# Performance work log

Measured on AMD Instinct MI355X. Metric: run time of the kernel, lower is better.

Reference implementation:

```python
import jax, jax.numpy as jnp
import numpy as np

K = 3          # opt.k: number of nearest SOM nodes each point is assigned to
SOM_M = 256    # opt.node_num (16x16 SOM grid)


def _point_resnet(x, ws, bs):
    # SO-Net PointResNet: stack of 1x1 conv (relu) layers; the LAST layer takes
    # concat(prev_out, input) as a residual skip connection.
    out = x
    n = len(ws)
    for i in range(n):
        inp = jnp.concatenate([out, x], axis=1) if i == n - 1 else out
        out = jax.nn.relu(jnp.einsum('oc,bcn->bon', ws[i], inp) + bs[i][None, :, None])
    return out


def _encoder(x, sn, node, fp_ws, fp_bs, fn_ws, fn_bs):
    B, _, N = x.shape
    M = node.shape[2]
    xd = jax.lax.stop_gradient(x)      # torch used x.data throughout SOM logic
    nd = jax.lax.stop_gradient(node)
    # squared distances point->node: B,N,M
    x2 = jnp.sum(xd * xd, axis=1)
    n2 = jnp.sum(nd * nd, axis=1)
    cross = jnp.einsum('bcn,bcm->bnm', xd, nd)
    d2 = x2[:, :, None] + n2[:, None, :] - 2.0 * cross
    _, knn_idx = jax.lax.top_k(-d2, K)                 # B,N,K nearest SOM nodes
    min_idx = jnp.transpose(knn_idx, (0, 2, 1)).reshape(B, K * N)  # B,kN (k-major, matches x_stack)
    x_stack = jnp.tile(x, (1, 1, K))                   # B,3,kN
    xs_d = jax.lax.stop_gradient(x_stack)
    # mask_row_sum (counts per node) and masked sum == one-hot mask multiply in the original
    counts = jax.vmap(lambda s: jax.ops.segment_sum(jnp.ones(s.shape, jnp.float32), s, num_segments=SOM_M))(min_idx)  # B,M
    sums = jax.vmap(lambda d, s: jax.ops.segment_sum(d, s, num_segments=SOM_M))(jnp.transpose(xs_d, (0, 2, 1)), min_idx)  # B,M,3
    cluster_mean = jnp.transpose(sums, (0, 2, 1)) / (counts[:, None, :] + 1e-5)  # B,3,M (new som_node)
    # centers: per-point gather of its assigned node (sum(mask*node) over M)
    centers = jnp.take_along_axis(cluster_mean, min_idx[:, None, :], axis=2)     # B,3,kN
    x_dec = jax.lax.stop_gradient(x_stack - centers)   # .detach() in original
    first = _point_resnet(x_dec, fp_ws, fp_bs)         # B,384,kN
    # index_max + gather: per (b,c,node) max over assigned points; empty nodes -> point index 0
    node_max = jax.vmap(lambda d, s: jax.ops.segment_max(d, s, num_segments=SOM_M))(jnp.transpose(first, (0, 2, 1)), min_idx)  # B,M,C
    node_max = jnp.transpose(node_max, (0, 2, 1))      # B,C,M
    has_pts = counts > 0                               # mask_row_max
    fallback = first[:, :, 0:1]                        # gather index 0 for empty nodes
    masked_max = jnp.where(has_pts[:, None, :], node_max, fallback)  # B,384,M
    final_in = jnp.concatenate([cluster_mean, masked_max], axis=1)   # B,387,M
    final = _point_resnet(final_in, fn_ws, fn_bs)      # B,1024,M
    return jnp.max(final, axis=2)                      # B,1024 global feature


def setup_inputs() -> dict:
    key = jax.random.key(0)
    ks = jax.random.split(key, 24)
    B, N, M = 8, 4096, SOM_M
    inp = {
        'x': jax.random.normal(ks[0], (B, 3, N), jnp.float32),
        'sn': jax.random.normal(ks[1], (B, 3, N), jnp.float32),
        'node': jax.random.normal(ks[2], (B, 3, M), jnp.float32),
        'node_knn_I': jax.random.randint(ks[3], (B, M, 1), 0, M),
    }
    fp_dims = [(3, 64), (64, 128), (128, 256), (256 + 3, 384)]
    fn_dims = [(387, 512), (512, 512), (512, 768), (768 + 387, 1024)]
    i = 4
    for j, (cin, cout) in enumerate(fp_dims):
        inp[f'fp_w{j}'] = jax.random.normal(ks[i], (cout, cin), jnp.float32) * np.float32(np.sqrt(2.0 / cin)); i += 1
        inp[f'fp_b{j}'] = jnp.zeros((cout,), jnp.float32)
    for j, (cin, cout) in enumerate(fn_dims):
        inp[f'fn_w{j}'] = jax.random.normal(ks[i], (cout, cin), jnp.float32) * np.float32(np.sqrt(2.0 / cin)); i += 1
        inp[f'fn_b{j}'] = jnp.zeros((cout,), jnp.float32)
    return inp


def reference(x, sn, node, node_knn_I,
              fp_w0, fp_b0, fp_w1, fp_b1, fp_w2, fp_b2, fp_w3, fp_b3,
              fn_w0, fn_b0, fn_w1, fn_b1, fn_w2, fn_b2, fn_w3, fn_b3):
    fp_ws = [fp_w0, fp_w1, fp_w2, fp_w3]
    fp_bs = [fp_b0, fp_b1, fp_b2, fp_b3]
    fn_ws = [fn_w0, fn_w1, fn_w2, fn_w3]
    fn_bs = [fn_b0, fn_b1, fn_b2, fn_b3]
    # node_knn_I only used when som_k >= 2 (KNNModule); som_k=1 here.
    return _encoder(x, sn, node, fp_ws, fp_bs, fn_ws, fn_bs)
```

## Files before the change

### kernel.cpp

```cpp
#include <hip/hip_runtime.h>
#include <math.h>

#define B_   8
#define N_   4096
#define M_   256
#define KNN_ 3

#define OFF_COUNTS   0
#define OFF_SUMS     2048
#define OFF_CM       8192
#define OFF_NODEMAX  14336
#define OFF_H0       14336
#define OFF_FIRST0   800768
#define OFF_CURSOR   803840
#define ZERO_COUNT   805888
#define OFF_OFFS     805888
#define OFF_KNN      807944
#define OFF_CAT      807944
#define OFF_SORTED   906248
#define OFF_MSORT    1004552
#define OFF_FIN2     2020360
#define OFF_H1       2020360
#define OFF_WBF      2544648
#define OFF_W3X      3661832
#define O_W0 0
#define O_W1 2048
#define O_W2 10240
#define O_W3 43008
#define O_V0 153600
#define O_V1 366592
#define O_V2 628736
#define O_V3 1021952
#define W_TOTAL 2234368

typedef short  bf16x8 __attribute__((ext_vector_type(8)));
typedef float  f32x4  __attribute__((ext_vector_type(4)));
typedef float  f32x16 __attribute__((ext_vector_type(16)));

__device__ __forceinline__ unsigned short f2b(float f) {
    unsigned u = __float_as_uint(f);
    return (unsigned short)((u + 0x7FFFu + ((u >> 16) & 1u)) >> 16);
}
__device__ __forceinline__ unsigned cvt2(float lo, float hi) {
    unsigned r;
    asm("v_cvt_pk_bf16_f32 %0, %1, %2" : "=v"(r) : "v"(lo), "v"(hi));
    return r;
}
__device__ __forceinline__ f32x16 zero16() {
    f32x16 z;
    #pragma unroll
    for (int i = 0; i < 16; i++) z[i] = 0.f;
    return z;
}

__global__ __launch_bounds__(256) void knn_setup(
        const float* __restrict__ x, const float* __restrict__ node,
        int* __restrict__ knn, float* __restrict__ counts, float* __restrict__ sums,
        const float* s0, const float* s1, const float* s2, const float* s3,
        const float* s4, const float* s5, const float* s6, const float* s7,
        unsigned short* __restrict__ dst, float* __restrict__ w3x) {
    __shared__ float nd0[M_], nd1[M_], nd2[M_], nn2[M_];
    int t = threadIdx.x;
    if (blockIdx.x < 128) {
        int b = blockIdx.x >> 4, xblk = blockIdx.x & 15;
        {
            float c0 = node[(b * 3 + 0) * M_ + t];
            float c1 = node[(b * 3 + 1) * M_ + t];
            float c2 = node[(b * 3 + 2) * M_ + t];
            nd0[t] = c0; nd1[t] = c1; nd2[t] = c2;
            nn2[t] = c0 * c0 + c1 * c1 + c2 * c2;
        }
        __syncthreads();
        int n = xblk * 256 + t;
        float x0 = x[(b * 3 + 0) * N_ + n];
        float x1 = x[(b * 3 + 1) * N_ + n];
        float x2 = x[(b * 3 + 2) * N_ + n];
        float xx = x0 * x0 + x1 * x1 + x2 * x2;
        float d0 = 1e30f, d1 = 1e30f, d2b = 1e30f;
        int i0 = 0, i1 = 0, i2 = 0;
        for (int m = 0; m < M_; m++) {
            float cross = x0 * nd0[m] + x1 * nd1[m] + x2 * nd2[m];
            float d = xx + nn2[m] - 2.f * cross;
            bool c0 = d < d0, c1 = d < d1, c2 = d < d2b;
            d2b = c1 ? d1 : (c2 ? d : d2b);
            i2  = c1 ? i1 : (c2 ? m : i2);
            d1  = c0 ? d0 : (c1 ? d : d1);
            i1  = c0 ? i0 : (c1 ? m : i1);
            d0  = c0 ? d  : d0;
            i0  = c0 ? m  : i0;
        }
        int base = (b * N_ + n) * 3;
        knn[base + 0] = i0; knn[base + 1] = i1; knn[base + 2] = i2;
        int mm[3] = {i0, i1, i2};
        #pragma unroll
        for (int k = 0; k < 3; k++) {
            int m = mm[k];
            atomicAdd(&counts[b * M_ + m], 1.f);
            atomicAdd(&sums[(b * M_ + m) * 3 + 0], x0);
            atomicAdd(&sums[(b * M_ + m) * 3 + 1], x1);
            atomicAdd(&sums[(b * M_ + m) * 3 + 2], x2);
        }
    } else {
        int i = (blockIdx.x - 128) * 256 + t;
        int st = (gridDim.x - 128) * 256;
        for (int j = i; j < 1536; j += st) {
            int ch = j >> 2, c = j & 3;
            w3x[j] = (c < 3) ? s3[ch * 259 + 256 + c] : 0.f;
        }
        for (; i < W_TOTAL; i += st) {
            const float* src; int base, cin, cinp;
            if      (i < O_W1) { src = s0; base = O_W0; cin = 3;    cinp = 32; }
            else if (i < O_W2) { src = s1; base = O_W1; cin = 64;   cinp = 64; }
            else if (i < O_W3) { src = s2; base = O_W2; cin = 128;  cinp = 128; }
            else if (i < O_V0) { src = s3; base = O_W3; cin = 259;  cinp = 288; }
            else if (i < O_V1) { src = s4; base = O_V0; cin = 387;  cinp = 416; }
            else if (i < O_V2) { src = s5; base = O_V1; cin = 512;  cinp = 512; }
            else if (i < O_V3) { src = s6; base = O_V2; cin = 512;  cinp = 512; }
            else               { src = s7; base = O_V3; cin = 1155; cinp = 1184; }
            int loc = i - base;
            int co = loc / cinp, k = loc - co * cinp;
            dst[i] = (k < cin) ? f2b(src[co * cin + k]) : (unsigned short)0;
        }
    }
}

__global__ __launch_bounds__(256) void cmean_scan(const float* __restrict__ counts,
        const float* __restrict__ sums, float* __restrict__ cm, int* __restrict__ offs) {
    __shared__ int tmp[256];
    int t = threadIdx.x, b = blockIdx.x;
    float cnt = counts[b * M_ + t];
    float inv = 1.f / (cnt + 1e-5f);
    #pragma unroll
    for (int c = 0; c < 3; c++)
        cm[(b * 3 + c) * M_ + t] = sums[(b * M_ + t) * 3 + c] * inv;
    int v = (int)cnt;
    tmp[t] = v;
    __syncthreads();
    for (int off = 1; off < 256; off <<= 1) {
        int u = (t >= off) ? tmp[t - off] : 0;
        __syncthreads();
        tmp[t] += u;
        __syncthreads();
    }
    offs[b * 257 + t] = tmp[t] - v;
    if (t == 255) offs[b * 257 + 256] = tmp[255];
}

__global__ __launch_bounds__(256) void scatter(const int* __restrict__ knn,
        const int* __restrict__ offs, int* __restrict__ cursor,
        int* __restrict__ sorted, int* __restrict__ msort) {
    int g = blockIdx.x * 256 + threadIdx.x;
    int b = g / (KNN_ * N_), j = g % (KNN_ * N_);
    int n = j & (N_ - 1), k = j >> 12;
    int m = knn[(b * N_ + n) * 3 + k];
    int pos = atomicAdd(&cursor[b * M_ + m], 1);
    int dst = offs[b * 257 + m] + pos;
    sorted[b * (KNN_ * N_) + dst] = j;
    msort[b * (KNN_ * N_) + dst] = m;
}

template<int KS, int INS, int OUTS, int CTW>
__device__ __forceinline__ void layerB(const unsigned short* __restrict__ Wg,
        const float* __restrict__ bias, const unsigned short* actin,
        unsigned short* actout, int wave, int lane) {
    int r = lane & 15, g = lane >> 4;
    bf16x8 bfr[4][KS];
    #pragma unroll
    for (int pt = 0; pt < 4; pt++) {
        const unsigned short* arow = actin + (pt * 16 + r) * INS + g * 8;
        #pragma unroll
        for (int ks = 0; ks < KS; ks++)
            bfr[pt][ks] = *(const bf16x8*)(arow + ks * 32);
    }
    #pragma unroll
    for (int c = 0; c < CTW; c++) {
        int ct = wave * CTW + c;
        const unsigned short* wrow = Wg + (ct * 16 + r) * (KS * 32) + g * 8;
        f32x4 acc[4];
        #pragma unroll
        for (int pt = 0; pt < 4; pt++) acc[pt] = (f32x4){0.f, 0.f, 0.f, 0.f};
        #pragma unroll
        for (int ks = 0; ks < KS; ks++) {
            bf16x8 wv = *(const bf16x8*)(wrow + ks * 32);
            #pragma unroll
            for (int pt = 0; pt < 4; pt++)
                acc[pt] = __builtin_amdgcn_mfma_f32_16x16x32_bf16(wv, bfr[pt][ks], acc[pt], 0, 0, 0);
        }
        f32x4 b4 = *(const f32x4*)(bias + ct * 16 + g * 4);
        #pragma unroll
        for (int pt = 0; pt < 4; pt++) {
            uint2 s;
            s.x = cvt2(fmaxf(acc[pt][0] + b4[0], 0.f), fmaxf(acc[pt][1] + b4[1], 0.f));
            s.y = cvt2(fmaxf(acc[pt][2] + b4[2], 0.f), fmaxf(acc[pt][3] + b4[3], 0.f));
            *(uint2*)(actout + (pt * 16 + r) * OUTS + ct * 16 + g * 4) = s;
        }
    }
}

__global__ __launch_bounds__(256, 3) void mlp1m(
        const float* __restrict__ x, const float* __restrict__ cm,
        const int* __restrict__ sorted, const int* __restrict__ msort,
        const unsigned short* __restrict__ wb, const float4* __restrict__ w3x,
        const float* __restrict__ bb0, const float* __restrict__ bb1,
        const float* __restrict__ bb2, const float* __restrict__ bb3,
        float* __restrict__ node_max, float* __restrict__ first0) {
    __shared__ __align__(16) char smem[50688];
    unsigned short* inb = (unsigned short*)smem;
    unsigned short* a1  = (unsigned short*)smem;
    unsigned short* a0  = (unsigned short*)(smem + 16896);
    unsigned short* cat = (unsigned short*)(smem + 16896);
    __shared__ float4 xdf[64];
    __shared__ int segm[65], segstart[66];
    __shared__ int nseg, p0loc;
    int t = threadIdx.x, b = blockIdx.y, lane = t & 63, wave = t >> 6;
    int e0 = blockIdx.x * 64;
    for (int e = t; e < 1280; e += 256) ((unsigned*)inb)[e] = 0u;
    __syncthreads();
    if (t < 64) {
        int p = t;
        if (p == 0) p0loc = -1;
        int j = sorted[b * 12288 + e0 + p];
        int m = msort[b * 12288 + e0 + p];
        int n = j & (N_ - 1);
        float xd0 = x[(b * 3 + 0) * N_ + n] - cm[(b * 3 + 0) * M_ + m];
        float xd1 = x[(b * 3 + 1) * N_ + n] - cm[(b * 3 + 1) * M_ + m];
        float xd2 = x[(b * 3 + 2) * N_ + n] - cm[(b * 3 + 2) * M_ + m];
        xdf[p] = make_float4(xd0, xd1, xd2, 0.f);
        inb[p * 40 + 0] = f2b(xd0);
        inb[p * 40 + 1] = f2b(xd1);
        inb[p * 40 + 2] = f2b(xd2);
        int prev = __shfl_up(m, 1);
        bool flag = (p == 0) || (m != prev);
        unsigned long long mk = __ballot(flag);
        int sid = __popcll(mk & ((1ull << p) - 1ull));
        if (flag) { segstart[sid] = p; segm[sid] = m; }
        if (p == 63) { int ns2 = __popcll(mk); nseg = ns2; segstart[ns2] = 64; }
        if (j == 0) p0loc = p;
    }
    __syncthreads();
    layerB<1, 40, 72, 1>(wb + O_W0, bb0, inb, a0, wave, lane);
    __syncthreads();
    layerB<2, 72, 132, 2>(wb + O_W1, bb1, a0, a1, wave, lane);
    __syncthreads();
    layerB<4, 132, 264, 4>(wb + O_W2, bb2, a1, cat, wave, lane);
    __syncthreads();
    int l31 = lane & 31, half = lane >> 5;
    f32x16 acc[6];
    #pragma unroll
    for (int q = 0; q < 6; q++) acc[q] = zero16();
    {
        const unsigned short* arow0 = cat + l31 * 264 + half * 8;
        const unsigned short* arow1 = cat + (32 + l31) * 264 + half * 8;
        const unsigned short* wrowb = wb + O_W3 + (wave * 96 + l31) * 288 + half * 8;
        #pragma unroll
        for (int ks = 0; ks < 16; ks++) {
            bf16x8 aA = *(const bf16x8*)(arow0 + ks * 16);
            bf16x8 aB = *(const bf16x8*)(arow1 + ks * 16);
            #pragma unroll
            for (int c3 = 0; c3 < 3; c3++) {
                bf16x8 wv = *(const bf16x8*)(wrowb + c3 * 32 * 288 + ks * 16);
                acc[c3 * 2 + 0] = __builtin_amdgcn_mfma_f32_32x32x16_bf16(aA, wv, acc[c3 * 2 + 0], 0, 0, 0);
                acc[c3 * 2 + 1] = __builtin_amdgcn_mfma_f32_32x32x16_bf16(aB, wv, acc[c3 * 2 + 1], 0, 0, 0);
            }
        }
    }
    int ns = nseg, p0l = p0loc;
    float bias3[3]; float4 wx3[3];
    #pragma unroll
    for (int c3 = 0; c3 < 3; c3++) {
        bias3[c3] = bb3[(wave * 3 + c3) * 32 + l31];
        wx3[c3]   = w3x[(wave * 3 + c3) * 32 + l31];
    }
    #pragma unroll
    for (int ph = 0; ph < 2; ph++) {
        #pragma unroll
        for (int rg = 0; rg < 16; rg++) {
            int row = ph * 32 + (rg & 3) + 8 * (rg >> 2) + 4 * half;
            float4 xv = xdf[row];
            #pragma unroll
            for (int c3 = 0; c3 < 3; c3++) {
                float s = acc[c3 * 2 + ph][rg] + bias3[c3]
                        + wx3[c3].x * xv.x + wx3[c3].y * xv.y + wx3[c3].z * xv.z;
                acc[c3 * 2 + ph][rg] = fmaxf(s, 0.f);
            }
        }
    }
    if (p0l >= 0) {
        #pragma unroll
        for (int ph = 0; ph < 2; ph++)
            #pragma unroll
            for (int rg = 0; rg < 16; rg++) {
                int row = ph * 32 + (rg & 3) + 8 * (rg >> 2) + 4 * half;
                if (row == p0l) {
                    #pragma unroll
                    for (int c3 = 0; c3 < 3; c3++)
                        first0[b * 384 + (wave * 3 + c3) * 32 + l31] = acc[c3 * 2 + ph][rg];
                }
            }
    }
    for (int s = 0; s < ns; s++) {
        int s0 = segstart[s], s1 = segstart[s + 1];
        float m0 = 0.f, m1 = 0.f, m2 = 0.f;
        if (s0 < 32) {
            #pragma unroll
            for (int rg = 0; rg < 16; rg++) {
                int row = (rg & 3) + 8 * (rg >> 2) + 4 * half;
                bool in = (row >= s0) && (row < s1);
                m0 = fmaxf(m0, in ? acc[0][rg] : 0.f);
                m1 = fmaxf(m1, in ? acc[2][rg] : 0.f);
                m2 = fmaxf(m2, in ? acc[4][rg] : 0.f);
            }
        }
        if (s1 > 32) {
            #pragma unroll
            for (int rg = 0; rg < 16; rg++) {
                int row = 32 + (rg & 3) + 8 * (rg >> 2) + 4 * half;
                bool in = (row >= s0) && (row < s1);
                m0 = fmaxf(m0, in ? acc[1][rg] : 0.f);
                m1 = fmaxf(m1, in ? acc[3][rg] : 0.f);
                m2 = fmaxf(m2, in ? acc[5][rg] : 0.f);
            }
        }
        m0 = fmaxf(m0, __shfl_xor(m0, 32));
        m1 = fmaxf(m1, __shfl_xor(m1, 32));
        m2 = fmaxf(m2, __shfl_xor(m2, 32));
        if (lane < 32) {
            float* dstp = &node_max[(size_t)(b * M_ + segm[s]) * 384 + wave * 96];
            atomicMax((int*)(dstp + l31),      __float_as_int(m0));
            atomicMax((int*)(dstp + 32 + l31), __float_as_int(m1));
            atomicMax((int*)(dstp + 64 + l31), __float_as_int(m2));
        }
    }
}

__global__ void build_fin2(const float* __restrict__ cm, const float* __restrict__ counts,
                           const float* __restrict__ nmax, const float* __restrict__ first0,
                           unsigned short* __restrict__ fin2, unsigned short* __restrict__ cat) {
    int tot = 2048 * 416;
    int i = blockIdx.x * blockDim.x + threadIdx.x;
    int st = gridDim.x * blockDim.x;
    for (; i < tot; i += st) {
        int n = i / 416, ch = i - n * 416;
        int b = n >> 8, m = n & 255;
        float v = 0.f;
        if (ch < 3) v = cm[(b * 3 + ch) * M_ + m];
        else if (ch < 387)
            v = (counts[n] > 0.f) ? nmax[(size_t)n * 384 + (ch - 3)]
                                  : first0[b * 384 + (ch - 3)];
        unsigned short u = f2b(v);
        fin2[n * 416 + ch] = u;
        cat[(size_t)n * 1184 + 768 + ch] = u;
    }
}

template<int KS, int CTQ>
__global__ __launch_bounds__(256, 2) void nlayer4(const unsigned short* __restrict__ W,
        const float* __restrict__ bias, const unsigned short* __restrict__ actin,
        unsigned short* __restrict__ actout, int outs) {
    int wave = threadIdx.x >> 6, lane = threadIdx.x & 63;
    int id = blockIdx.x * 4 + wave;
    int nt = id / CTQ, cq = id - nt * CTQ;
    int r = lane & 15, g = lane >> 4;
    const unsigned short* arow = actin + (size_t)(nt * 16 + r) * (KS * 32) + g * 8;
    bf16x8 afr[KS];
    #pragma unroll
    for (int ks = 0; ks < KS; ks++) afr[ks] = *(const bf16x8*)(arow + ks * 32);
    const unsigned short* w0 = W + (cq * 64 + r) * (KS * 32) + g * 8;
    f32x4 acc[4];
    #pragma unroll
    for (int c = 0; c < 4; c++) acc[c] = (f32x4){0.f, 0.f, 0.f, 0.f};
    #pragma unroll
    for (int ks = 0; ks < KS; ks++) {
        #pragma unroll
        for (int c = 0; c < 4; c++) {
            bf16x8 wv = *(const bf16x8*)(w0 + c * 16 * KS * 32 + ks * 32);
            acc[c] = __builtin_amdgcn_mfma_f32_16x16x32_bf16(wv, afr[ks], acc[c], 0, 0, 0);
        }
    }
    #pragma unroll
    for (int c = 0; c < 4; c++) {
        f32x4 b4 = *(const f32x4*)(bias + cq * 64 + c * 16 + g * 4);
        uint2 s;
        s.x = cvt2(fmaxf(acc[c][0] + b4[0], 0.f), fmaxf(acc[c][1] + b4[1], 0.f));
        s.y = cvt2(fmaxf(acc[c][2] + b4[2], 0.f), fmaxf(acc[c][3] + b4[3], 0.f));
        *(uint2*)(actout + (size_t)(nt * 16 + r) * outs + cq * 64 + c * 16 + g * 4) = s;
    }
}

__global__ __launch_bounds__(256) void nlayer_max_s(const unsigned short* __restrict__ W,
        const float* __restrict__ bias, const unsigned short* __restrict__ actin,
        float* __restrict__ out) {
    int wave = threadIdx.x >> 6, lane = threadIdx.x & 63;
    int id = blockIdx.x * 4 + wave;
    int nt = id >> 5, cp = id & 31;
    int r = lane & 15, g = lane >> 4;
    const unsigned short* arow = actin + (size_t)(nt * 16 + r) * 1184 + g * 8;
    const unsigned short* w0 = W + (size_t)(cp * 32 + r) * 1184 + g * 8;
    const unsigned short* w1 = w0 + 16 * 1184;
    f32x4 a0 = {0.f, 0.f, 0.f, 0.f}, a1 = {0.f, 0.f, 0.f, 0.f};
    #pragma unroll 4
    for (int ks = 0; ks < 37; ks++) {
        bf16x8 av = *(const bf16x8*)(arow + ks * 32);
        a0 = __builtin_amdgcn_mfma_f32_16x16x32_bf16(*(const bf16x8*)(w0 + ks * 32), av, a0, 0, 0, 0);
        a1 = __builtin_amdgcn_mfma_f32_16x16x32_bf16(*(const bf16x8*)(w1 + ks * 32), av, a1, 0, 0, 0);
    }
    int b = nt >> 4;
    #pragma unroll
    for (int c = 0; c < 2; c++) {
        f32x4 acc = c ? a1 : a0;
        f32x4 b4 = *(const f32x4*)(bias + cp * 32 + c * 16 + g * 4);
        #pragma unroll
        for (int i = 0; i < 4; i++) {
            float v = fmaxf(acc[i] + b4[i], 0.f);
            v = fmaxf(v, __shfl_xor(v, 1));
            v = fmaxf(v, __shfl_xor(v, 2));
            v = fmaxf(v, __shfl_xor(v, 4));
            v = fmaxf(v, __shfl_xor(v, 8));
            if (r == 0)
                atomicMax((int*)&out[b * 1024 + cp * 32 + c * 16 + g * 4 + i],
                          __float_as_int(v));
        }
    }
}

extern "C" void kernel_launch(void* const* d_in, const int* in_sizes, int n_in,
                              void* d_out, int out_size, void* d_ws, size_t ws_size,
                              hipStream_t stream) {
    (void)in_sizes; (void)n_in; (void)out_size; (void)ws_size;
    const float* x    = (const float*)d_in[0];
    const float* node = (const float*)d_in[2];
    const float* fpw[4] = {(const float*)d_in[4], (const float*)d_in[6],
                           (const float*)d_in[8], (const float*)d_in[10]};
    const float* fpb[4] = {(const float*)d_in[5], (const float*)d_in[7],
                           (const float*)d_in[9], (const float*)d_in[11]};
    const float* fnw[4] = {(const float*)d_in[12], (const float*)d_in[14],
                           (const float*)d_in[16], (const float*)d_in[18]};
    const float* fnb[4] = {(const float*)d_in[13], (const float*)d_in[15],
                           (const float*)d_in[17], (const float*)d_in[19]};
    float* ws  = (float*)d_ws;
    float* out = (float*)d_out;
    unsigned short* wb   = (unsigned short*)(ws + OFF_WBF);
    unsigned short* fin2 = (unsigned short*)(ws + OFF_FIN2);
    unsigned short* h0   = (unsigned short*)(ws + OFF_H0);
    unsigned short* h1   = (unsigned short*)(ws + OFF_H1);
    unsigned short* catb = (unsigned short*)(ws + OFF_CAT);

    hipMemsetAsync(ws, 0, (size_t)ZERO_COUNT * 4, stream);
    hipMemsetAsync(out, 0, (size_t)B_ * 1024 * 4, stream);

    knn_setup<<<128 + 2048, 256, 0, stream>>>(
        x, node, (int*)(ws + OFF_KNN), ws + OFF_COUNTS, ws + OFF_SUMS,
        fpw[0], fpw[1], fpw[2], fpw[3], fnw[0], fnw[1], fnw[2], fnw[3],
        wb, ws + OFF_W3X);
    cmean_scan<<<B_, 256, 0, stream>>>(
        ws + OFF_COUNTS, ws + OFF_SUMS, ws + OFF_CM, (int*)(ws + OFF_OFFS));
    scatter<<<B_ * KNN_ * N_ / 256, 256, 0, stream>>>(
        (int*)(ws + OFF_KNN), (int*)(ws + OFF_OFFS), (int*)(ws + OFF_CURSOR),
        (int*)(ws + OFF_SORTED), (int*)(ws + OFF_MSORT));
    mlp1m<<<dim3(KNN_ * N_ / 64, B_), 256, 0, stream>>>(
        x, ws + OFF_CM, (int*)(ws + OFF_SORTED), (int*)(ws + OFF_MSORT), wb,
        (const float4*)(ws + OFF_W3X),
        fpb[0], fpb[1], fpb[2], fpb[3], ws + OFF_NODEMAX, ws + OFF_FIRST0);
    build_fin2<<<3328, 256, 0, stream>>>(
        ws + OFF_CM, ws + OFF_COUNTS, ws + OFF_NODEMAX, ws + OFF_FIRST0, fin2, catb);
    nlayer4<13, 8><<<256,  256, 0, stream>>>(wb + O_V0, fnb[0], fin2, h0, 512);
    nlayer4<16, 8><<<256,  256, 0, stream>>>(wb + O_V1, fnb[1], h0, h1, 512);
    nlayer4<16, 12><<<384, 256, 0, stream>>>(wb + O_V2, fnb[2], h1, catb, 1184);
    nlayer_max_s<<<1024, 256, 0, stream>>>(wb + O_V3, fnb[3], catb, out);
}
```

Baseline: 193.8 us.

## Fuse node MLP layers into one LDS-resident kernel and merge scan with scatter

Replaces build_fin2, three nlayer4 launches and nlayer_max_s with a single node_mlp kernel. Each 1024-thread block handles 16 nodes and keeps the intermediate activations in shared memory, so they never round-trip through global memory. Also folds the scatter into the prefix-scan kernel using shared-memory cursors, which removes a launch and the global atomics. The cost is much less parallelism: only 128 blocks for the node MLP and 8 blocks for the scatter, and every block re-reads the full weights from global or L2.

```diff
diff --git a/kernel.cpp b/kernel.cpp
--- a/kernel.cpp
+++ b/kernel.cpp
@@ -10,17 +10,11 @@
 #define OFF_SUMS     2048
 #define OFF_CM       8192
 #define OFF_NODEMAX  14336
-#define OFF_H0       14336
 #define OFF_FIRST0   800768
-#define OFF_CURSOR   803840
-#define ZERO_COUNT   805888
-#define OFF_OFFS     805888
+#define ZERO_COUNT   803840
 #define OFF_KNN      807944
-#define OFF_CAT      807944
 #define OFF_SORTED   906248
 #define OFF_MSORT    1004552
-#define OFF_FIN2     2020360
-#define OFF_H1       2020360
 #define OFF_WBF      2544648
 #define OFF_W3X      3661832
 #define O_W0 0
@@ -124,9 +118,10 @@
     }
 }
 
-__global__ __launch_bounds__(256) void cmean_scan(const float* __restrict__ counts,
-        const float* __restrict__ sums, float* __restrict__ cm, int* __restrict__ offs) {
-    __shared__ int tmp[256];
+__global__ __launch_bounds__(256) void prep(const float* __restrict__ counts,
+        const float* __restrict__ sums, const int* __restrict__ knn,
+        float* __restrict__ cm, int* __restrict__ sorted, int* __restrict__ msort) {
+    __shared__ int tmp[256], offsL[257], cur[256];
     int t = threadIdx.x, b = blockIdx.x;
     float cnt = counts[b * M_ + t];
     float inv = 1.f / (cnt + 1e-5f);
@@ -134,7 +129,7 @@
     for (int c = 0; c < 3; c++)
         cm[(b * 3 + c) * M_ + t] = sums[(b * M_ + t) * 3 + c] * inv;
     int v = (int)cnt;
-    tmp[t] = v;
+    tmp[t] = v; cur[t] = 0;
     __syncthreads();
     for (int off = 1; off < 256; off <<= 1) {
         int u = (t >= off) ? tmp[t - off] : 0;
@@ -142,21 +137,17 @@
         tmp[t] += u;
         __syncthreads();
     }
-    offs[b * 257 + t] = tmp[t] - v;
-    if (t == 255) offs[b * 257 + 256] = tmp[255];
-}
-
-__global__ __launch_bounds__(256) void scatter(const int* __restrict__ knn,
-        const int* __restrict__ offs, int* __restrict__ cursor,
-        int* __restrict__ sorted, int* __restrict__ msort) {
-    int g = blockIdx.x * 256 + threadIdx.x;
-    int b = g / (KNN_ * N_), j = g % (KNN_ * N_);
-    int n = j & (N_ - 1), k = j >> 12;
-    int m = knn[(b * N_ + n) * 3 + k];
-    int pos = atomicAdd(&cursor[b * M_ + m], 1);
-    int dst = offs[b * 257 + m] + pos;
-    sorted[b * (KNN_ * N_) + dst] = j;
-    msort[b * (KNN_ * N_) + dst] = m;
+    offsL[t] = tmp[t] - v;
+    if (t == 255) offsL[256] = tmp[255];
+    __syncthreads();
+    for (int e = t; e < KNN_ * N_; e += 256) {
+        int n = e & (N_ - 1), k = e >> 12;
+        int m = knn[(b * N_ + n) * 3 + k];
+        int pos = atomicAdd(&cur[m], 1);
+        int dst = offsL[m] + pos;
+        sorted[b * (KNN_ * N_) + dst] = e;
+        msort[b * (KNN_ * N_) + dst] = m;
+    }
 }
 
 template<int KS, int INS, int OUTS, int CTW>
@@ -333,92 +324,134 @@
     }
 }
 
-__global__ void build_fin2(const float* __restrict__ cm, const float* __restrict__ counts,
-                           const float* __restrict__ nmax, const float* __restrict__ first0,
-                           unsigned short* __restrict__ fin2, unsigned short* __restrict__ cat) {
-    int tot = 2048 * 416;
-    int i = blockIdx.x * blockDim.x + threadIdx.x;
-    int st = gridDim.x * blockDim.x;
-    for (; i < tot; i += st) {
-        int n = i / 416, ch = i - n * 416;
-        int b = n >> 8, m = n & 255;
+__global__ __launch_bounds__(1024) void node_mlp(
+        const float* __restrict__ cm, const float* __restrict__ counts,
+        const float* __restrict__ nmax, const float* __restrict__ first0,
+        const unsigned short* __restrict__ wb,
+        const float* __restrict__ q0, const float* __restrict__ q1,
+        const float* __restrict__ q2, const float* __restrict__ q3,
+        float* __restrict__ out) {
+    __shared__ __align__(16) char smem[71424];
+    unsigned short* cat = (unsigned short*)smem;
+    unsigned short* h0  = (unsigned short*)(smem + 38144);
+    unsigned short* h1  = (unsigned short*)(smem + 54784);
+    int t = threadIdx.x, lane = t & 63, w = t >> 6;
+    int nt = blockIdx.x, b = nt >> 4;
+    for (int e = t; e < 16 * 424; e += 1024) {
+        int nl = e / 424, ch = e - nl * 424;
+        int ng = nt * 16 + nl, m = ng & 255;
         float v = 0.f;
         if (ch < 3) v = cm[(b * 3 + ch) * M_ + m];
         else if (ch < 387)
-            v = (counts[n] > 0.f) ? nmax[(size_t)n * 384 + (ch - 3)]
-                                  : first0[b * 384 + (ch - 3)];
-        unsigned short u = f2b(v);
-        fin2[n * 416 + ch] = u;
-        cat[(size_t)n * 1184 + 768 + ch] = u;
-    }
-}
-
-template<int KS, int CTQ>
-__global__ __launch_bounds__(256, 2) void nlayer4(const unsigned short* __restrict__ W,
-        const float* __restrict__ bias, const unsigned short* __restrict__ actin,
-        unsigned short* __restrict__ actout, int outs) {
-    int wave = threadIdx.x >> 6, lane = threadIdx.x & 63;
-    int id = blockIdx.x * 4 + wave;
-    int nt = id / CTQ, cq = id - nt * CTQ;
+            v = (counts[ng] > 0.f) ? nmax[(size_t)ng * 384 + (ch - 3)]
+                                   : first0[b * 384 + (ch - 3)];
+        cat[nl * 1192 + 768 + ch] = f2b(v);
+    }
+    __syncthreads();
     int r = lane & 15, g = lane >> 4;
-    const unsigned short* arow = actin + (size_t)(nt * 16 + r) * (KS * 32) + g * 8;
-    bf16x8 afr[KS];
-    #pragma unroll
-    for (int ks = 0; ks < KS; ks++) afr[ks] = *(const bf16x8*)(arow + ks * 32);
-    const unsigned short* w0 = W + (cq * 64 + r) * (KS * 32) + g * 8;
-    f32x4 acc[4];
-    #pragma unroll
-    for (int c = 0; c < 4; c++) acc[c] = (f32x4){0.f, 0.f, 0.f, 0.f};
-    #pragma unroll
-    for (int ks = 0; ks < KS; ks++) {
+    {
+        bf16x8 afr[13];
+        const unsigned short* arow = cat + r * 1192 + 768 + g * 8;
+        #pragma unroll
+        for (int ks = 0; ks < 13; ks++) afr[ks] = *(const bf16x8*)(arow + ks * 32);
+        f32x4 acc[2] = {{0.f,0.f,0.f,0.f}, {0.f,0.f,0.f,0.f}};
+        const unsigned short* w0 = wb + O_V0 + ((w * 2) * 16 + r) * 416 + g * 8;
+        #pragma unroll
+        for (int ks = 0; ks < 13; ks++) {
+            #pragma unroll
+            for (int c = 0; c < 2; c++)
+                acc[c] = __builtin_amdgcn_mfma_f32_16x16x32_bf16(
+                    *(const bf16x8*)(w0 + c * 16 * 416 + ks * 32), afr[ks], acc[c], 0, 0, 0);
+        }
+        #pragma unroll
+        for (int c = 0; c < 2; c++) {
+            int ct = w * 2 + c;
+            f32x4 b4 = *(const f32x4*)(q0 + ct * 16 + g * 4);
+            uint2 s;
+            s.x = cvt2(fmaxf(acc[c][0] + b4[0], 0.f), fmaxf(acc[c][1] + b4[1], 0.f));
+            s.y = cvt2(fmaxf(acc[c][2] + b4[2], 0.f), fmaxf(acc[c][3] + b4[3], 0.f));
+            *(uint2*)(h0 + r * 520 + ct * 16 + g * 4) = s;
+        }
+    }
+    __syncthreads();
+    {
+        bf16x8 afr[16];
+        const unsigned short* arow = h0 + r * 520 + g * 8;
+        #pragma unroll
+        for (int ks = 0; ks < 16; ks++) afr[ks] = *(const bf16x8*)(arow + ks * 32);
+        f32x4 acc[2] = {{0.f,0.f,0.f,0.f}, {0.f,0.f,0.f,0.f}};
+        const unsigned short* w0 = wb + O_V1 + ((w * 2) * 16 + r) * 512 + g * 8;
+        #pragma unroll
+        for (int ks = 0; ks < 16; ks++) {
+            #pragma unroll
+            for (int c = 0; c < 2; c++)
+                acc[c] = __builtin_amdgcn_mfma_f32_16x16x32_bf16(
+                    *(const bf16x8*)(w0 + c * 16 * 512 + ks * 32), afr[ks], acc[c], 0, 0, 0);
+        }
+        #pragma unroll
+        for (int c = 0; c < 2; c++) {
+            int ct = w * 2 + c;
+            f32x4 b4 = *(const f32x4*)(q1 + ct * 16 + g * 4);
+            uint2 s;
+            s.x = cvt2(fmaxf(acc[c][0] + b4[0], 0.f), fmaxf(acc[c][1] + b4[1], 0.f));
+            s.y = cvt2(fmaxf(acc[c][2] + b4[2], 0.f), fmaxf(acc[c][3] + b4[3], 0.f));
+            *(uint2*)(h1 + r * 520 + ct * 16 + g * 4) = s;
+        }
+    }
+    __syncthreads();
+    {
+        bf16x8 afr[16];
+        const unsigned short* arow = h1 + r * 520 + g * 8;
+        #pragma unroll
+        for (int ks = 0; ks < 16; ks++) afr[ks] = *(const bf16x8*)(arow + ks * 32);
+        f32x4 acc[3] = {{0.f,0.f,0.f,0.f}, {0.f,0.f,0.f,0.f}, {0.f,0.f,0.f,0.f}};
+        const unsigned short* w0 = wb + O_V2 + ((w * 3) * 16 + r) * 512 + g * 8;
+        #pragma unroll
+        for (int ks = 0; ks < 16; ks++) {
+            #pragma unroll
+            for (int c = 0; c < 3; c++)
+                acc[c] = __builtin_amdgcn_mfma_f32_16x16x32_bf16(
+                    *(const bf16x8*)(w0 + c * 16 * 512 + ks * 32), afr[ks], acc[c], 0, 0, 0);
+        }
+        #pragma unroll
+        for (int c = 0; c < 3; c++) {
+            int ct = w * 3 + c;
+            f32x4 b4 = *(const f32x4*)(q2 + ct * 16 + g * 4);
+            uint2 s;
+            s.x = cvt2(fmaxf(acc[c][0] + b4[0], 0.f), fmaxf(acc[c][1] + b4[1], 0.f));
+            s.y = cvt2(fmaxf(acc[c][2] + b4[2], 0.f), fmaxf(acc[c][3] + b4[3], 0.f));
+            *(uint2*)(cat + r * 1192 + ct * 16 + g * 4) = s;
+        }
+    }
+    __syncthreads();
+    {
+        f32x4 acc[4] = {{0.f,0.f,0.f,0.f}, {0.f,0.f,0.f,0.f},
+                        {0.f,0.f,0.f,0.f}, {0.f,0.f,0.f,0.f}};
+        const unsigned short* arow = cat + r * 1192 + g * 8;
+        const unsigned short* w0 = wb + O_V3 + (size_t)((w * 4) * 16 + r) * 1184 + g * 8;
+        #pragma unroll 4
+        for (int ks = 0; ks < 37; ks++) {
+            bf16x8 av = *(const bf16x8*)(arow + ks * 32);
+            #pragma unroll
+            for (int c = 0; c < 4; c++)
+                acc[c] = __builtin_amdgcn_mfma_f32_16x16x32_bf16(
+                    *(const bf16x8*)(w0 + (size_t)c * 16 * 1184 + ks * 32), av, acc[c], 0, 0, 0);
+        }
         #pragma unroll
         for (int c = 0; c < 4; c++) {
-            bf16x8 wv = *(const bf16x8*)(w0 + c * 16 * KS * 32 + ks * 32);
-            acc[c] = __builtin_amdgcn_mfma_f32_16x16x32_bf16(wv, afr[ks], acc[c], 0, 0, 0);
-        }
-    }
-    #pragma unroll
-    for (int c = 0; c < 4; c++) {
-        f32x4 b4 = *(const f32x4*)(bias + cq * 64 + c * 16 + g * 4);
-        uint2 s;
-        s.x = cvt2(fmaxf(acc[c][0] + b4[0], 0.f), fmaxf(acc[c][1] + b4[1], 0.f));
-        s.y = cvt2(fmaxf(acc[c][2] + b4[2], 0.f), fmaxf(acc[c][3] + b4[3], 0.f));
-        *(uint2*)(actout + (size_t)(nt * 16 + r) * outs + cq * 64 + c * 16 + g * 4) = s;
-    }
-}
-
-__global__ __launch_bounds__(256) void nlayer_max_s(const unsigned short* __restrict__ W,
-        const float* __restrict__ bias, const unsigned short* __restrict__ actin,
-        float* __restrict__ out) {
-    int wave = threadIdx.x >> 6, lane = threadIdx.x & 63;
-    int id = blockIdx.x * 4 + wave;
-    int nt = id >> 5, cp = id & 31;
-    int r = lane & 15, g = lane >> 4;
-    const unsigned short* arow = actin + (size_t)(nt * 16 + r) * 1184 + g * 8;
-    const unsigned short* w0 = W + (size_t)(cp * 32 + r) * 1184 + g * 8;
-    const unsigned short* w1 = w0 + 16 * 1184;
-    f32x4 a0 = {0.f, 0.f, 0.f, 0.f}, a1 = {0.f, 0.f, 0.f, 0.f};
-    #pragma unroll 4
-    for (int ks = 0; ks < 37; ks++) {
-        bf16x8 av = *(const bf16x8*)(arow + ks * 32);
-        a0 = __builtin_amdgcn_mfma_f32_16x16x32_bf16(*(const bf16x8*)(w0 + ks * 32), av, a0, 0, 0, 0);
-        a1 = __builtin_amdgcn_mfma_f32_16x16x32_bf16(*(const bf16x8*)(w1 + ks * 32), av, a1, 0, 0, 0);
-    }
-    int b = nt >> 4;
-    #pragma unroll
-    for (int c = 0; c < 2; c++) {
-        f32x4 acc = c ? a1 : a0;
-        f32x4 b4 = *(const f32x4*)(bias + cp * 32 + c * 16 + g * 4);
-        #pragma unroll
-        for (int i = 0; i < 4; i++) {
-            float v = fmaxf(acc[i] + b4[i], 0.f);
-            v = fmaxf(v, __shfl_xor(v, 1));
-            v = fmaxf(v, __shfl_xor(v, 2));
-            v = fmaxf(v, __shfl_xor(v, 4));
-            v = fmaxf(v, __shfl_xor(v, 8));
-            if (r == 0)
-                atomicMax((int*)&out[b * 1024 + cp * 32 + c * 16 + g * 4 + i],
-                          __float_as_int(v));
+            int ct = w * 4 + c;
+            f32x4 b4 = *(const f32x4*)(q3 + ct * 16 + g * 4);
+            #pragma unroll
+            for (int i = 0; i < 4; i++) {
+                float v = fmaxf(acc[c][i] + b4[i], 0.f);
+                v = fmaxf(v, __shfl_xor(v, 1));
+                v = fmaxf(v, __shfl_xor(v, 2));
+                v = fmaxf(v, __shfl_xor(v, 4));
+                v = fmaxf(v, __shfl_xor(v, 8));
+                if (r == 0)
+                    atomicMax((int*)&out[b * 1024 + ct * 16 + g * 4 + i],
+                              __float_as_int(v));
+            }
         }
     }
 }
@@ -439,11 +472,7 @@
                            (const float*)d_in[17], (const float*)d_in[19]};
     float* ws  = (float*)d_ws;
     float* out = (float*)d_out;
-    unsigned short* wb   = (unsigned short*)(ws + OFF_WBF);
-    unsigned short* fin2 = (unsigned short*)(ws + OFF_FIN2);
-    unsigned short* h0   = (unsigned short*)(ws + OFF_H0);
-    unsigned short* h1   = (unsigned short*)(ws + OFF_H1);
-    unsigned short* catb = (unsigned short*)(ws + OFF_CAT);
+    unsigned short* wb = (unsigned short*)(ws + OFF_WBF);
 
     hipMemsetAsync(ws, 0, (size_t)ZERO_COUNT * 4, stream);
     hipMemsetAsync(out, 0, (size_t)B_ * 1024 * 4, stream);
@@ -452,19 +481,14 @@
         x, node, (int*)(ws + OFF_KNN), ws + OFF_COUNTS, ws + OFF_SUMS,
         fpw[0], fpw[1], fpw[2], fpw[3], fnw[0], fnw[1], fnw[2], fnw[3],
         wb, ws + OFF_W3X);
-    cmean_scan<<<B_, 256, 0, stream>>>(
-        ws + OFF_COUNTS, ws + OFF_SUMS, ws + OFF_CM, (int*)(ws + OFF_OFFS));
-    scatter<<<B_ * KNN_ * N_ / 256, 256, 0, stream>>>(
-        (int*)(ws + OFF_KNN), (int*)(ws + OFF_OFFS), (int*)(ws + OFF_CURSOR),
-        (int*)(ws + OFF_SORTED), (int*)(ws + OFF_MSORT));
+    prep<<<B_, 256, 0, stream>>>(
+        ws + OFF_COUNTS, ws + OFF_SUMS, (int*)(ws + OFF_KNN),
+        ws + OFF_CM, (int*)(ws + OFF_SORTED), (int*)(ws + OFF_MSORT));
     mlp1m<<<dim3(KNN_ * N_ / 64, B_), 256, 0, stream>>>(
         x, ws + OFF_CM, (int*)(ws + OFF_SORTED), (int*)(ws + OFF_MSORT), wb,
         (const float4*)(ws + OFF_W3X),
         fpb[0], fpb[1], fpb[2], fpb[3], ws + OFF_NODEMAX, ws + OFF_FIRST0);
-    build_fin2<<<3328, 256, 0, stream>>>(
-        ws + OFF_CM, ws + OFF_COUNTS, ws + OFF_NODEMAX, ws + OFF_FIRST0, fin2, catb);
-    nlayer4<13, 8><<<256,  256, 0, stream>>>(wb + O_V0, fnb[0], fin2, h0, 512);
-    nlayer4<16, 8><<<256,  256, 0, stream>>>(wb + O_V1, fnb[1], h0, h1, 512);
-    nlayer4<16, 12><<<384, 256, 0, stream>>>(wb + O_V2, fnb[2], h1, catb, 1184);
-    nlayer_max_s<<<1024, 256, 0, stream>>>(wb + O_V3, fnb[3], catb, out);
-}
+    node_mlp<<<128, 1024, 0, stream>>>(
+        ws + OFF_CM, ws + OFF_COUNTS, ws + OFF_NODEMAX, ws + OFF_FIRST0, wb,
+        fnb[0], fnb[1], fnb[2], fnb[3], out);
+}
```

Result: slower. 225.9 us (+16.5%).

## Fuse cluster-mean, scan and scatter into one per-batch kernel with LDS atomics

Applied to the files above, without the earlier changes.

Removes the global atomic accumulation of counts and sums from the KNN kernel and merges the cmean_scan and scatter kernels into a single per-batch prep kernel. The new kernel builds histograms and coordinate sums with shared-memory atomics, runs the prefix scan, and scatters into sorted order using LDS cursors. It also specializes the weight-conversion loop with shifts instead of generic division, and shrinks the workspace memset to only the node-max region. This removes two launches and global atomic contention, but the prep kernel runs on only 8 blocks and serially walks 12288 elements per block, which may lengthen the critical path.

```diff
diff --git a/kernel.cpp b/kernel.cpp
--- a/kernel.cpp
+++ b/kernel.cpp
@@ -7,14 +7,10 @@
 #define KNN_ 3
 
 #define OFF_COUNTS   0
-#define OFF_SUMS     2048
 #define OFF_CM       8192
 #define OFF_NODEMAX  14336
 #define OFF_H0       14336
 #define OFF_FIRST0   800768
-#define OFF_CURSOR   803840
-#define ZERO_COUNT   805888
-#define OFF_OFFS     805888
 #define OFF_KNN      807944
 #define OFF_CAT      807944
 #define OFF_SORTED   906248
@@ -55,7 +51,7 @@
 
 __global__ __launch_bounds__(256) void knn_setup(
         const float* __restrict__ x, const float* __restrict__ node,
-        int* __restrict__ knn, float* __restrict__ counts, float* __restrict__ sums,
+        int* __restrict__ knn,
         const float* s0, const float* s1, const float* s2, const float* s3,
         const float* s4, const float* s5, const float* s6, const float* s7,
         unsigned short* __restrict__ dst, float* __restrict__ w3x) {
@@ -91,15 +87,6 @@
         }
         int base = (b * N_ + n) * 3;
         knn[base + 0] = i0; knn[base + 1] = i1; knn[base + 2] = i2;
-        int mm[3] = {i0, i1, i2};
-        #pragma unroll
-        for (int k = 0; k < 3; k++) {
-            int m = mm[k];
-            atomicAdd(&counts[b * M_ + m], 1.f);
-            atomicAdd(&sums[(b * M_ + m) * 3 + 0], x0);
-            atomicAdd(&sums[(b * M_ + m) * 3 + 1], x1);
-            atomicAdd(&sums[(b * M_ + m) * 3 + 2], x2);
-        }
     } else {
         int i = (blockIdx.x - 128) * 256 + t;
         int st = (gridDim.x - 128) * 256;
@@ -108,32 +95,62 @@
             w3x[j] = (c < 3) ? s3[ch * 259 + 256 + c] : 0.f;
         }
         for (; i < W_TOTAL; i += st) {
-            const float* src; int base, cin, cinp;
-            if      (i < O_W1) { src = s0; base = O_W0; cin = 3;    cinp = 32; }
-            else if (i < O_W2) { src = s1; base = O_W1; cin = 64;   cinp = 64; }
-            else if (i < O_W3) { src = s2; base = O_W2; cin = 128;  cinp = 128; }
-            else if (i < O_V0) { src = s3; base = O_W3; cin = 259;  cinp = 288; }
-            else if (i < O_V1) { src = s4; base = O_V0; cin = 387;  cinp = 416; }
-            else if (i < O_V2) { src = s5; base = O_V1; cin = 512;  cinp = 512; }
-            else if (i < O_V3) { src = s6; base = O_V2; cin = 512;  cinp = 512; }
-            else               { src = s7; base = O_V3; cin = 1155; cinp = 1184; }
-            int loc = i - base;
-            int co = loc / cinp, k = loc - co * cinp;
-            dst[i] = (k < cin) ? f2b(src[co * cin + k]) : (unsigned short)0;
-        }
-    }
-}
-
-__global__ __launch_bounds__(256) void cmean_scan(const float* __restrict__ counts,
-        const float* __restrict__ sums, float* __restrict__ cm, int* __restrict__ offs) {
-    __shared__ int tmp[256];
+            unsigned short v;
+            if (i < O_W1) {
+                int loc = i, co = loc >> 5, k = loc & 31;
+                v = (k < 3) ? f2b(s0[co * 3 + k]) : (unsigned short)0;
+            } else if (i < O_W2) {
+                int loc = i - O_W1, co = loc >> 6, k = loc & 63;
+                v = f2b(s1[co * 64 + k]);
+            } else if (i < O_W3) {
+                int loc = i - O_W2, co = loc >> 7, k = loc & 127;
+                v = f2b(s2[co * 128 + k]);
+            } else if (i < O_V0) {
+                int loc = i - O_W3, co = loc / 288u, k = loc - co * 288;
+                v = (k < 259) ? f2b(s3[co * 259 + k]) : (unsigned short)0;
+            } else if (i < O_V1) {
+                int loc = i - O_V0, co = loc / 416u, k = loc - co * 416;
+                v = (k < 387) ? f2b(s4[co * 387 + k]) : (unsigned short)0;
+            } else if (i < O_V2) {
+                int loc = i - O_V1, co = loc >> 9, k = loc & 511;
+                v = f2b(s5[co * 512 + k]);
+            } else if (i < O_V3) {
+                int loc = i - O_V2, co = loc >> 9, k = loc & 511;
+                v = f2b(s6[co * 512 + k]);
+            } else {
+                int loc = i - O_V3, co = loc / 1184u, k = loc - co * 1184;
+                v = (k < 1155) ? f2b(s7[co * 1155 + k]) : (unsigned short)0;
+            }
+            dst[i] = v;
+        }
+    }
+}
+
+__global__ __launch_bounds__(256) void prep(const float* __restrict__ x,
+        const int* __restrict__ knn, float* __restrict__ counts_g,
+        float* __restrict__ cm, int* __restrict__ sorted, int* __restrict__ msort) {
+    __shared__ float hs0[256], hs1[256], hs2[256];
+    __shared__ int hc[256], tmp[256], offsL[257], cur[256];
     int t = threadIdx.x, b = blockIdx.x;
-    float cnt = counts[b * M_ + t];
+    hs0[t] = 0.f; hs1[t] = 0.f; hs2[t] = 0.f; hc[t] = 0; cur[t] = 0;
+    __syncthreads();
+    for (int e = t; e < KNN_ * N_; e += 256) {
+        int n = e & (N_ - 1), k = e >> 12;
+        int m = knn[(b * N_ + n) * 3 + k];
+        (void)k;
+        atomicAdd(&hc[m], 1);
+        atomicAdd(&hs0[m], x[(b * 3 + 0) * N_ + n]);
+        atomicAdd(&hs1[m], x[(b * 3 + 1) * N_ + n]);
+        atomicAdd(&hs2[m], x[(b * 3 + 2) * N_ + n]);
+    }
+    __syncthreads();
+    int v = hc[t];
+    float cnt = (float)v;
+    counts_g[b * M_ + t] = cnt;
     float inv = 1.f / (cnt + 1e-5f);
-    #pragma unroll
-    for (int c = 0; c < 3; c++)
-        cm[(b * 3 + c) * M_ + t] = sums[(b * M_ + t) * 3 + c] * inv;
-    int v = (int)cnt;
+    cm[(b * 3 + 0) * M_ + t] = hs0[t] * inv;
+    cm[(b * 3 + 1) * M_ + t] = hs1[t] * inv;
+    cm[(b * 3 + 2) * M_ + t] = hs2[t] * inv;
     tmp[t] = v;
     __syncthreads();
     for (int off = 1; off < 256; off <<= 1) {
@@ -142,21 +159,17 @@
         tmp[t] += u;
         __syncthreads();
     }
-    offs[b * 257 + t] = tmp[t] - v;
-    if (t == 255) offs[b * 257 + 256] = tmp[255];
-}
-
-__global__ __launch_bounds__(256) void scatter(const int* __restrict__ knn,
-        const int* __restrict__ offs, int* __restrict__ cursor,
-        int* __restrict__ sorted, int* __restrict__ msort) {
-    int g = blockIdx.x * 256 + threadIdx.x;
-    int b = g / (KNN_ * N_), j = g % (KNN_ * N_);
-    int n = j & (N_ - 1), k = j >> 12;
-    int m = knn[(b * N_ + n) * 3 + k];
-    int pos = atomicAdd(&cursor[b * M_ + m], 1);
-    int dst = offs[b * 257 + m] + pos;
-    sorted[b * (KNN_ * N_) + dst] = j;
-    msort[b * (KNN_ * N_) + dst] = m;
+    offsL[t] = tmp[t] - v;
+    if (t == 255) offsL[256] = tmp[255];
+    __syncthreads();
+    for (int e = t; e < KNN_ * N_; e += 256) {
+        int n = e & (N_ - 1), k = e >> 12;
+        int m = knn[(b * N_ + n) * 3 + k];
+        int pos = atomicAdd(&cur[m], 1);
+        int dst = offsL[m] + pos;
+        sorted[b * (KNN_ * N_) + dst] = e;
+        msort[b * (KNN_ * N_) + dst] = m;
+    }
 }
 
 template<int KS, int INS, int OUTS, int CTW>
@@ -445,18 +458,16 @@
     unsigned short* h1   = (unsigned short*)(ws + OFF_H1);
     unsigned short* catb = (unsigned short*)(ws + OFF_CAT);
 
-    hipMemsetAsync(ws, 0, (size_t)ZERO_COUNT * 4, stream);
+    hipMemsetAsync(ws + OFF_NODEMAX, 0, (size_t)(B_ * M_ * 384) * 4, stream);
     hipMemsetAsync(out, 0, (size_t)B_ * 1024 * 4, stream);
 
     knn_setup<<<128 + 2048, 256, 0, stream>>>(
-        x, node, (int*)(ws + OFF_KNN), ws + OFF_COUNTS, ws + OFF_SUMS,
+        x, node, (int*)(ws + OFF_KNN),
         fpw[0], fpw[1], fpw[2], fpw[3], fnw[0], fnw[1], fnw[2], fnw[3],
         wb, ws + OFF_W3X);
-    cmean_scan<<<B_, 256, 0, stream>>>(
-        ws + OFF_COUNTS, ws + OFF_SUMS, ws + OFF_CM, (int*)(ws + OFF_OFFS));
-    scatter<<<B_ * KNN_ * N_ / 256, 256, 0, stream>>>(
-        (int*)(ws + OFF_KNN), (int*)(ws + OFF_OFFS), (int*)(ws + OFF_CURSOR),
-        (int*)(ws + OFF_SORTED), (int*)(ws + OFF_MSORT));
+    prep<<<B_, 256, 0, stream>>>(
+        x, (int*)(ws + OFF_KNN), ws + OFF_COUNTS,
+        ws + OFF_CM, (int*)(ws + OFF_SORTED), (int*)(ws + OFF_MSORT));
     mlp1m<<<dim3(KNN_ * N_ / 64, B_), 256, 0, stream>>>(
         x, ws + OFF_CM, (int*)(ws + OFF_SORTED), (int*)(ws + OFF_MSORT), wb,
         (const float4*)(ws + OFF_W3X),
```

Result: slower. 236.5 us (+22.0%).
